# Kernel optimization log

Measured on AMD Instinct MI355X. Metric: run time of the kernel, lower is better.

The kernel has to match this reference:

```python
import jax, jax.numpy as jnp
import numpy as np

D_MODEL = 1024
H = 16
DK = D_MODEL // H
B, S = 2, 2048
NEG = -1e9


def setup_inputs() -> dict:
    key = jax.random.key(0)
    ks = jax.random.split(key, 7)
    scale = 1.0 / np.sqrt(D_MODEL)
    inp = {
        "q": jax.random.normal(ks[0], (B, S, D_MODEL), jnp.float32),
        "k": jax.random.normal(ks[1], (B, S, D_MODEL), jnp.float32),
        "v": jax.random.normal(ks[2], (B, S, D_MODEL), jnp.float32),
        # causal mask, broadcastable to (B, H, S, S); positions with 0 are masked
        "mask": jnp.tril(jnp.ones((S, S), dtype=bool))[None, None, :, :],
        "w_q": jax.random.normal(ks[3], (D_MODEL, D_MODEL), jnp.float32) * scale,
        "w_k": jax.random.normal(ks[4], (D_MODEL, D_MODEL), jnp.float32) * scale,
        "w_v": jax.random.normal(ks[5], (D_MODEL, D_MODEL), jnp.float32) * scale,
        "w_o": jax.random.normal(ks[6], (D_MODEL, D_MODEL), jnp.float32) * scale,
    }
    return inp


def reference(q, k, v, mask, w_q, w_k, w_v, w_o):
    # Linear projections (nn.Linear with bias=False: x @ W.T)
    query = q @ w_q.T  # (B, S, d_model)
    key_ = k @ w_k.T
    value = v @ w_v.T
    # split heads -> (B, h, S, dk)
    def split(x):
        return x.reshape(x.shape[0], x.shape[1], H, DK).transpose(0, 2, 1, 3)
    qh, kh, vh = split(query), split(key_), split(value)
    # scaled dot-product attention with full score materialization
    scores = jnp.einsum("bhqd,bhkd->bhqk", qh, kh) / jnp.sqrt(jnp.float32(DK))
    scores = jnp.where(mask, scores, NEG)
    attn = jax.nn.softmax(scores, axis=-1)  # (B, h, S, S); dropout p=0.0 -> identity
    out = jnp.einsum("bhqk,bhkd->bhqd", attn, vh)
    # merge heads -> (B, S, d_model)
    out = out.transpose(0, 2, 1, 3).reshape(out.shape[0], -1, H * DK)
    return out @ w_o.T
```

## Files before the change

### kernel.cpp

```cpp
#include <hip/hip_runtime.h>
#include <cstdint>
#include <cstddef>

typedef __bf16 bf16;
typedef __attribute__((ext_vector_type(4))) __bf16 bf16x4;
typedef __attribute__((ext_vector_type(8))) __bf16 bf16x8;
typedef __attribute__((ext_vector_type(4))) float floatx4;
typedef __attribute__((ext_vector_type(4))) short short4v;

#define MFMA16(a, b, c) __builtin_amdgcn_mfma_f32_16x16x32_bf16((a), (b), (c), 0, 0, 0)

__device__ __forceinline__ floatx4 MFMAK16(bf16x4 a, bf16x4 b, floatx4 c) {
#if __has_builtin(__builtin_amdgcn_mfma_f32_16x16x16bf16_1k)
  return __builtin_amdgcn_mfma_f32_16x16x16bf16_1k(
      __builtin_bit_cast(short4v, a), __builtin_bit_cast(short4v, b), c, 0, 0, 0);
#else
  floatx4 d;
  asm("v_mfma_f32_16x16x16_bf16 %0, %1, %2, %3"
      : "=v"(d)
      : "v"(a), "v"(b), "v"(c));
  return d;
#endif
}

constexpr int DMODEL = 1024;
constexpr int NH = 16;
constexpr int DKH = 64;
constexpr int B_ = 2;
constexpr int S_ = 2048;
constexpr int MTOT = B_ * S_;
constexpr float CEXP = 0.125f * 1.44269504f;

__device__ __forceinline__ void load_lds16(const void* g, void* l) {
  __builtin_amdgcn_global_load_lds(
      (const __attribute__((address_space(1))) uint32_t*)g,
      (__attribute__((address_space(3))) uint32_t*)l, 16, 0, 0);
}

__device__ __forceinline__ bf16x8 frag64(const bf16* lds, int row, int p) {
  int s = p ^ (row & 7);
  return *(const bf16x8*)&lds[row * 64 + s * 8];
}
__device__ __forceinline__ bf16x4 frag64h(const bf16* lds, int row, int p, int h) {
  int s = p ^ (row & 7);
  return *(const bf16x4*)&lds[row * 64 + s * 8 + h * 4];
}

__device__ __forceinline__ void stage32_bf16(const bf16* __restrict__ src,
                                             bf16* lds, int wave, int lane,
                                             int ldg) {
#pragma unroll
  for (int i = 0; i < 2; ++i) {
    int cb = (wave * 2 + i) * 64;
    int c = cb + lane;
    int r = c >> 2;
    int s = (c & 3) ^ ((r >> 1) & 3);
    load_lds16(&src[(size_t)r * ldg + s * 8], &lds[cb * 8]);
  }
}
__device__ __forceinline__ bf16x8 frag32_bf16(const bf16* lds, int row,
                                              int quad) {
  int s = quad ^ ((row >> 1) & 3);
  return *(const bf16x8*)&lds[row * 32 + s * 8];
}
__device__ __forceinline__ void stage32_f32(const float* __restrict__ src,
                                            float* lds, int wave, int lane,
                                            int ldg) {
#pragma unroll
  for (int i = 0; i < 4; ++i) {
    int cb = (wave * 4 + i) * 64;
    int c = cb + lane;
    int r = c >> 3;
    int s = (c & 7) ^ (r & 7);
    load_lds16(&src[(size_t)r * ldg + s * 4], &lds[cb * 4]);
  }
}
__device__ __forceinline__ bf16x8 frag32_f32(const float* lds, int row,
                                             int quad) {
  int s1 = (2 * quad) ^ (row & 7);
  int s2 = (2 * quad + 1) ^ (row & 7);
  float4 a = *(const float4*)&lds[row * 32 + s1 * 4];
  float4 b = *(const float4*)&lds[row * 32 + s2 * 4];
  bf16x8 h = {(bf16)a.x, (bf16)a.y, (bf16)a.z, (bf16)a.w,
              (bf16)b.x, (bf16)b.y, (bf16)b.z, (bf16)b.w};
  return h;
}

__global__ __launch_bounds__(256) void convert_kernel(
    const float* __restrict__ q, const float* __restrict__ k,
    const float* __restrict__ v, const float* __restrict__ wq,
    const float* __restrict__ wk, const float* __restrict__ wv,
    const float* __restrict__ wo, bf16* __restrict__ qb, bf16* __restrict__ kb,
    bf16* __restrict__ vb, bf16* __restrict__ wqb, bf16* __restrict__ wkb,
    bf16* __restrict__ wvb, bf16* __restrict__ wob) {
  const float* src;
  bf16* dst;
  size_t n;
  switch (blockIdx.y) {
    case 0: src = q;  dst = qb;  n = (size_t)MTOT * DMODEL; break;
    case 1: src = k;  dst = kb;  n = (size_t)MTOT * DMODEL; break;
    case 2: src = v;  dst = vb;  n = (size_t)MTOT * DMODEL; break;
    case 3: src = wq; dst = wqb; n = (size_t)DMODEL * DMODEL; break;
    case 4: src = wk; dst = wkb; n = (size_t)DMODEL * DMODEL; break;
    case 5: src = wv; dst = wvb; n = (size_t)DMODEL * DMODEL; break;
    default: src = wo; dst = wob; n = (size_t)DMODEL * DMODEL; break;
  }
  size_t idx = ((size_t)blockIdx.x * 256 + threadIdx.x) * 8;
  if (idx >= n) return;
  float4 f0 = *(const float4*)&src[idx];
  float4 f1 = *(const float4*)&src[idx + 4];
  bf16x8 h = {(bf16)f0.x, (bf16)f0.y, (bf16)f0.z, (bf16)f0.w,
              (bf16)f1.x, (bf16)f1.y, (bf16)f1.z, (bf16)f1.w};
  *(bf16x8*)&dst[idx] = h;
}

template <typename TC>
__device__ __forceinline__ void gemm64(const bf16* __restrict__ A,
                                       const bf16* __restrict__ W,
                                       TC* __restrict__ C,
                                       bf16* __restrict__ vt, int K,
                                       int m0, int n0, float ascale) {
  constexpr int N = DMODEL;
  __shared__ alignas(16) bf16 As[128 * 64];
  __shared__ alignas(16) bf16 Bs[128 * 64];

  const int tid = threadIdx.x;
  const int wave = tid >> 6;
  const int lane = tid & 63;
  const int quad = lane >> 4;
  const int l16 = lane & 15;
  const int wm = (wave >> 1) * 64;
  const int wn = (wave & 1) * 64;

  floatx4 acc[4][4] = {};

  for (int k0 = 0; k0 < K; k0 += 64) {
#pragma unroll
    for (int i = 0; i < 4; ++i) {
      int cb = (wave * 4 + i) * 64;
      int c = cb + lane;
      int r = c >> 3;
      int s = (c & 7) ^ (r & 7);
      load_lds16(&A[(size_t)(m0 + r) * K + k0 + s * 8], &As[cb * 8]);
      load_lds16(&W[(size_t)(n0 + r) * K + k0 + s * 8], &Bs[cb * 8]);
    }
    __syncthreads();

#pragma unroll
    for (int kk = 0; kk < 2; ++kk) {
      bf16x8 af[4], bfv[4];
#pragma unroll
      for (int mi = 0; mi < 4; ++mi)
        af[mi] = frag64(As, wm + mi * 16 + l16, kk * 4 + quad);
#pragma unroll
      for (int ni = 0; ni < 4; ++ni)
        bfv[ni] = frag64(Bs, wn + ni * 16 + l16, kk * 4 + quad);
#pragma unroll
      for (int mi = 0; mi < 4; ++mi)
#pragma unroll
        for (int ni = 0; ni < 4; ++ni)
          acc[mi][ni] = MFMA16(af[mi], bfv[ni], acc[mi][ni]);
    }
    __syncthreads();
  }

  if (vt) {
#pragma unroll
    for (int mi = 0; mi < 4; ++mi)
#pragma unroll
      for (int ni = 0; ni < 4; ++ni)
#pragma unroll
        for (int r = 0; r < 4; ++r) {
          int row = m0 + wm + mi * 16 + quad * 4 + r;
          int col = n0 + wn + ni * 16 + l16;
          int bb = row >> 11, s = row & 2047;
          int h = col >> 6, d = col & 63;
          vt[(size_t)((bb * NH + h) * DKH + d) * S_ + s] = (bf16)acc[mi][ni][r];
        }
  } else {
#pragma unroll
    for (int mi = 0; mi < 4; ++mi)
#pragma unroll
      for (int ni = 0; ni < 4; ++ni)
#pragma unroll
        for (int r = 0; r < 4; ++r) {
          int row = m0 + wm + mi * 16 + quad * 4 + r;
          int col = n0 + wn + ni * 16 + l16;
          C[(size_t)row * N + col] = (TC)(acc[mi][ni][r] * ascale);
        }
  }
}

__global__ __launch_bounds__(256, 3) void qkv64_kernel(
    const bf16* __restrict__ q, const bf16* __restrict__ k,
    const bf16* __restrict__ v, const bf16* __restrict__ wq,
    const bf16* __restrict__ wk, const bf16* __restrict__ wv,
    bf16* __restrict__ Q, bf16* __restrict__ K, bf16* __restrict__ Vt) {
  const int bid = blockIdx.x;
  const int xcd = bid & 7;
  const int j = bid >> 3;
  const int n = j & 7;
  const int rowslot = j >> 3;
  const int p = xcd * 12 + rowslot;
  const int z = p >> 5;
  const int y = p & 31;

  const bf16* A = (z == 0) ? q : (z == 1) ? k : v;
  const bf16* W = (z == 0) ? wq : (z == 1) ? wk : wv;
  bf16* C = (z == 0) ? Q : K;
  gemm64<bf16>(A, W, (z == 2) ? nullptr : C, (z == 2) ? Vt : nullptr,
               DMODEL, y * 128, n * 128, (z == 0) ? CEXP : 1.0f);
}

__global__ __launch_bounds__(256) void oproj64_kernel(
    const bf16* __restrict__ A, const bf16* __restrict__ W,
    float* __restrict__ C) {
  constexpr int K = DMODEL;
  constexpr int N = DMODEL;
  __shared__ alignas(16) bf16 As[64 * 64];
  __shared__ alignas(16) bf16 Bs[128 * 64];

  const int bid = blockIdx.x;
  const int xcd = bid & 7;
  const int j = bid >> 3;
  const int n = j & 7;
  const int slot = j >> 3;
  const int mt = xcd * 8 + slot;
  const int m0 = mt * 64;
  const int n0 = n * 128;

  const int tid = threadIdx.x;
  const int wave = tid >> 6;
  const int lane = tid & 63;
  const int quad = lane >> 4;
  const int l16 = lane & 15;
  const int wm = (wave >> 1) * 32;
  const int wn = (wave & 1) * 64;

  floatx4 acc[2][4] = {};

  for (int k0 = 0; k0 < K; k0 += 64) {
#pragma unroll
    for (int i = 0; i < 2; ++i) {
      int cb = (wave * 2 + i) * 64;
      int c = cb + lane;
      int r = c >> 3;
      int s = (c & 7) ^ (r & 7);
      load_lds16(&A[(size_t)(m0 + r) * K + k0 + s * 8], &As[cb * 8]);
    }
#pragma unroll
    for (int i = 0; i < 4; ++i) {
      int cb = (wave * 4 + i) * 64;
      int c = cb + lane;
      int r = c >> 3;
      int s = (c & 7) ^ (r & 7);
      load_lds16(&W[(size_t)(n0 + r) * K + k0 + s * 8], &Bs[cb * 8]);
    }
    __syncthreads();

#pragma unroll
    for (int kk = 0; kk < 2; ++kk) {
      bf16x8 af[2], bfv[4];
#pragma unroll
      for (int mi = 0; mi < 2; ++mi)
        af[mi] = frag64(As, wm + mi * 16 + l16, kk * 4 + quad);
#pragma unroll
      for (int ni = 0; ni < 4; ++ni)
        bfv[ni] = frag64(Bs, wn + ni * 16 + l16, kk * 4 + quad);
#pragma unroll
      for (int mi = 0; mi < 2; ++mi)
#pragma unroll
        for (int ni = 0; ni < 4; ++ni)
          acc[mi][ni] = MFMA16(af[mi], bfv[ni], acc[mi][ni]);
    }
    __syncthreads();
  }

#pragma unroll
  for (int mi = 0; mi < 2; ++mi)
#pragma unroll
    for (int ni = 0; ni < 4; ++ni)
#pragma unroll
      for (int r = 0; r < 4; ++r) {
        int row = m0 + wm + mi * 16 + quad * 4 + r;
        int col = n0 + wn + ni * 16 + l16;
        C[(size_t)row * N + col] = acc[mi][ni][r];
      }
}

template <typename TA, typename TW, typename TC>
__device__ __forceinline__ void gemm_core(const TA* __restrict__ A,
                                          const TW* __restrict__ W,
                                          TC* __restrict__ C,
                                          bf16* __restrict__ vt, int K,
                                          int m0, int n0, float ascale) {
  constexpr int N = DMODEL;
  __shared__ alignas(16) char smem[128 * 32 * (sizeof(TA) + sizeof(TW))];
  TA* As = (TA*)smem;
  TW* Bs = (TW*)(smem + 128 * 32 * sizeof(TA));

  const int tid = threadIdx.x;
  const int wave = tid >> 6;
  const int lane = tid & 63;
  const int quad = lane >> 4;
  const int l16 = lane & 15;
  const int wm = (wave >> 1) * 64;
  const int wn = (wave & 1) * 64;

  floatx4 acc[4][4] = {};

  for (int k0 = 0; k0 < K; k0 += 32) {
    if constexpr (sizeof(TA) == 2)
      stage32_bf16((const bf16*)A + (size_t)m0 * K + k0, (bf16*)As, wave, lane, K);
    else
      stage32_f32((const float*)A + (size_t)m0 * K + k0, (float*)As, wave, lane, K);
    if constexpr (sizeof(TW) == 2)
      stage32_bf16((const bf16*)W + (size_t)n0 * K + k0, (bf16*)Bs, wave, lane, K);
    else
      stage32_f32((const float*)W + (size_t)n0 * K + k0, (float*)Bs, wave, lane, K);
    __syncthreads();

    bf16x8 af[4], bfv[4];
#pragma unroll
    for (int mi = 0; mi < 4; ++mi) {
      if constexpr (sizeof(TA) == 2)
        af[mi] = frag32_bf16((const bf16*)As, wm + mi * 16 + l16, quad);
      else
        af[mi] = frag32_f32((const float*)As, wm + mi * 16 + l16, quad);
    }
#pragma unroll
    for (int ni = 0; ni < 4; ++ni) {
      if constexpr (sizeof(TW) == 2)
        bfv[ni] = frag32_bf16((const bf16*)Bs, wn + ni * 16 + l16, quad);
      else
        bfv[ni] = frag32_f32((const float*)Bs, wn + ni * 16 + l16, quad);
    }
#pragma unroll
    for (int mi = 0; mi < 4; ++mi)
#pragma unroll
      for (int ni = 0; ni < 4; ++ni)
        acc[mi][ni] = MFMA16(af[mi], bfv[ni], acc[mi][ni]);
    __syncthreads();
  }

  if (vt) {
#pragma unroll
    for (int mi = 0; mi < 4; ++mi)
#pragma unroll
      for (int ni = 0; ni < 4; ++ni)
#pragma unroll
        for (int r = 0; r < 4; ++r) {
          int row = m0 + wm + mi * 16 + quad * 4 + r;
          int col = n0 + wn + ni * 16 + l16;
          int bb = row >> 11, s = row & 2047;
          int h = col >> 6, d = col & 63;
          vt[(size_t)((bb * NH + h) * DKH + d) * S_ + s] = (bf16)acc[mi][ni][r];
        }
  } else {
#pragma unroll
    for (int mi = 0; mi < 4; ++mi)
#pragma unroll
      for (int ni = 0; ni < 4; ++ni)
#pragma unroll
        for (int r = 0; r < 4; ++r) {
          int row = m0 + wm + mi * 16 + quad * 4 + r;
          int col = n0 + wn + ni * 16 + l16;
          C[(size_t)row * N + col] = (TC)(acc[mi][ni][r] * ascale);
        }
  }
}

__global__ __launch_bounds__(256) void qkv_f32_kernel(
    const float* __restrict__ q, const float* __restrict__ k,
    const float* __restrict__ v, const float* __restrict__ wq,
    const float* __restrict__ wk, const float* __restrict__ wv,
    bf16* __restrict__ Q, bf16* __restrict__ K, bf16* __restrict__ Vt) {
  const int bid = blockIdx.x;
  const int xcd = bid & 7;
  const int j = bid >> 3;
  const int n = j & 7;
  const int rowslot = j >> 3;
  const int p = xcd * 12 + rowslot;
  const int z = p >> 5;
  const int y = p & 31;
  const float* A = (z == 0) ? q : (z == 1) ? k : v;
  const float* W = (z == 0) ? wq : (z == 1) ? wk : wv;
  bf16* C = (z == 0) ? Q : K;
  gemm_core<float, float, bf16>(A, W, (z == 2) ? nullptr : C,
                                (z == 2) ? Vt : nullptr, DMODEL, y * 128,
                                n * 128, (z == 0) ? CEXP : 1.0f);
}

__global__ __launch_bounds__(256) void oproj_f32_kernel(
    const bf16* __restrict__ A, const float* __restrict__ W,
    float* __restrict__ C) {
  const int bid = blockIdx.x;
  const int xcd = bid & 7;
  const int j = bid >> 3;
  const int n = j & 7;
  const int rowslot = j >> 3;
  const int y = xcd * 4 + rowslot;
  gemm_core<bf16, float, float>(A, W, C, nullptr, DMODEL, y * 128, n * 128,
                                1.0f);
}

__device__ __forceinline__ void stage_kv(const bf16* __restrict__ K,
                                         const bf16* __restrict__ Vt,
                                         bf16* Ks, bf16* Vts, size_t baseQ,
                                         size_t baseV, int kt, int wave,
                                         int lane) {
#pragma unroll
  for (int i = 0; i < 2; ++i) {
    int cb = (wave * 2 + i) * 64;
    int c = cb + lane;
    int r = c >> 3;
    int s = (c & 7) ^ (r & 7);
    load_lds16(&K[baseQ + (size_t)(kt * 64 + r) * DMODEL + s * 8], &Ks[cb * 8]);
    load_lds16(&Vt[baseV + (size_t)r * S_ + kt * 64 + s * 8], &Vts[cb * 8]);
  }
}

template <bool DIAG>
__device__ __forceinline__ void softmax4(const floatx4 sa[4], bf16x4 pb[4],
                                         float lp[4], int quad, int qb) {
#pragma unroll
  for (int kg = 0; kg < 4; ++kg) {
    float pv[4];
#pragma unroll
    for (int r = 0; r < 4; ++r) {
      float s = sa[kg][r];
      if (DIAG) {
        int key = kg * 16 + quad * 4 + r;
        s = (key > qb) ? -3.0e38f : s;
      }
      float p = __builtin_amdgcn_exp2f(s);
      lp[kg] += p;
      pv[r] = p;
    }
    pb[kg] = bf16x4{(bf16)pv[0], (bf16)pv[1], (bf16)pv[2], (bf16)pv[3]};
  }
}

template <bool DIAG>
__device__ __forceinline__ void attn_tile(const bf16* Ks, const bf16* Vts,
                                          const bf16x8 qf[2], floatx4 ot[4],
                                          float lp[4], int quad, int l16,
                                          int qb) {
  floatx4 sa[4] = {};
#pragma unroll
  for (int kk = 0; kk < 2; ++kk)
#pragma unroll
    for (int kg = 0; kg < 4; ++kg) {
      bf16x8 ka = frag64(Ks, kg * 16 + l16, kk * 4 + quad);
      sa[kg] = MFMA16(ka, qf[kk], sa[kg]);
    }
  bf16x4 pb[4];
  softmax4<DIAG>(sa, pb, lp, quad, qb);
#pragma unroll
  for (int kg = 0; kg < 4; ++kg)
#pragma unroll
    for (int di = 0; di < 4; ++di) {
      bf16x4 va = frag64h(Vts, di * 16 + l16, kg * 2 + (quad >> 1), quad & 1);
      ot[di] = MFMAK16(va, pb[kg], ot[di]);
    }
}

template <int LMODE>
__device__ __forceinline__ void pair_tile(const bf16* Ks, const bf16* Vts,
                                          const bf16x8 qfL[2],
                                          const bf16x8 qfH[2], floatx4 otL[4],
                                          floatx4 otH[4], float lpL[4],
                                          float lpH[4], int quad, int l16,
                                          int qb) {
  floatx4 saL[4] = {}, saH[4] = {};
#pragma unroll
  for (int kk = 0; kk < 2; ++kk)
#pragma unroll
    for (int kg = 0; kg < 4; ++kg) {
      bf16x8 ka = frag64(Ks, kg * 16 + l16, kk * 4 + quad);
      saL[kg] = MFMA16(ka, qfL[kk], saL[kg]);
      saH[kg] = MFMA16(ka, qfH[kk], saH[kg]);
    }
  bf16x4 pbL[4], pbH[4];
  if (LMODE == 1)
    softmax4<false>(saL, pbL, lpL, quad, qb);
  else
    softmax4<true>(saL, pbL, lpL, quad, qb);
  softmax4<false>(saH, pbH, lpH, quad, qb);
#pragma unroll
  for (int kg = 0; kg < 4; ++kg)
#pragma unroll
    for (int di = 0; di < 4; ++di) {
      bf16x4 va = frag64h(Vts, di * 16 + l16, kg * 2 + (quad >> 1), quad & 1);
      otL[di] = MFMAK16(va, pbL[kg], otL[di]);
      otH[di] = MFMAK16(va, pbH[kg], otH[di]);
    }
}

__global__ __launch_bounds__(256) void attn8_kernel(const bf16* __restrict__ Q,
                                                    const bf16* __restrict__ K,
                                                    const bf16* __restrict__ Vt,
                                                    bf16* __restrict__ O) {
  __shared__ alignas(16) bf16 Ks[2][64 * 64];
  __shared__ alignas(16) bf16 Vts[2][64 * 64];

  const int tid = threadIdx.x;
  const int wave = tid >> 6;
  const int lane = tid & 63;
  const int quad = lane >> 4;
  const int l16 = lane & 15;

  const int j = blockIdx.x;
  const int bh = j & 31;
  const int pr = j >> 5;
  const int qtL = pr;
  const int qtH = 31 - pr;
  const int h = bh & 15;
  const int b = bh >> 4;
  const size_t baseQ = (size_t)b * S_ * DMODEL + (size_t)h * DKH;
  const size_t baseV = (size_t)bh * DKH * S_;

  bf16x8 qfL[2], qfH[2];
#pragma unroll
  for (int kk = 0; kk < 2; ++kk) {
    qfL[kk] = *(const bf16x8*)&Q[baseQ +
        (size_t)(qtL * 64 + wave * 16 + l16) * DMODEL + kk * 32 + quad * 8];
    qfH[kk] = *(const bf16x8*)&Q[baseQ +
        (size_t)(qtH * 64 + wave * 16 + l16) * DMODEL + kk * 32 + quad * 8];
  }

  floatx4 otL[4] = {}, otH[4] = {};
  float lpL[4] = {}, lpH[4] = {};
  const int qb = wave * 16 + l16;

  stage_kv(K, Vt, Ks[0], Vts[0], baseQ, baseV, 0, wave, lane);
  __syncthreads();

  for (int kt = 0; kt < qtH; ++kt) {
    const int cur = kt & 1;
    stage_kv(K, Vt, Ks[cur ^ 1], Vts[cur ^ 1], baseQ, baseV, kt + 1, wave, lane);

    __builtin_amdgcn_s_setprio(1);
    if (kt < qtL)
      pair_tile<1>(Ks[cur], Vts[cur], qfL, qfH, otL, otH, lpL, lpH, quad, l16, qb);
    else if (kt == qtL)
      pair_tile<2>(Ks[cur], Vts[cur], qfL, qfH, otL, otH, lpL, lpH, quad, l16, qb);
    else
      attn_tile<false>(Ks[cur], Vts[cur], qfH, otH, lpH, quad, l16, qb);
    __builtin_amdgcn_s_setprio(0);

    __syncthreads();
  }
  {
    const int cur = qtH & 1;
    attn_tile<true>(Ks[cur], Vts[cur], qfH, otH, lpH, quad, l16, qb);
  }

  float lL = (lpL[0] + lpL[1]) + (lpL[2] + lpL[3]);
  lL += __shfl_xor(lL, 16, 64);
  lL += __shfl_xor(lL, 32, 64);
  float lH = (lpH[0] + lpH[1]) + (lpH[2] + lpH[3]);
  lH += __shfl_xor(lH, 16, 64);
  lH += __shfl_xor(lH, 32, 64);
  const float invL = 1.0f / lL;
  const float invH = 1.0f / lH;

  const size_t orowL = baseQ + (size_t)(qtL * 64 + wave * 16 + l16) * DMODEL;
  const size_t orowH = baseQ + (size_t)(qtH * 64 + wave * 16 + l16) * DMODEL;
#pragma unroll
  for (int di = 0; di < 4; ++di)
#pragma unroll
    for (int r = 0; r < 4; ++r) {
      O[orowL + di * 16 + quad * 4 + r] = (bf16)(otL[di][r] * invL);
      O[orowH + di * 16 + quad * 4 + r] = (bf16)(otH[di][r] * invH);
    }
}

extern "C" void kernel_launch(void* const* d_in, const int* in_sizes, int n_in,
                              void* d_out, int out_size, void* d_ws,
                              size_t ws_size, hipStream_t stream) {
  const float* q = (const float*)d_in[0];
  const float* k = (const float*)d_in[1];
  const float* v = (const float*)d_in[2];
  const float* wq = (const float*)d_in[4];
  const float* wk = (const float*)d_in[5];
  const float* wv = (const float*)d_in[6];
  const float* wo = (const float*)d_in[7];
  float* out = (float*)d_out;

  const size_t MB = 1024 * 1024;
  char* base = (char*)d_ws;
  bf16* Qp = (bf16*)(base);
  bf16* Kp = (bf16*)(base + 8 * MB);
  bf16* VtG = (bf16*)(base + 16 * MB);
  bf16* AO = (bf16*)(base + 24 * MB);

  if (ws_size >= 64 * MB) {
    bf16* qb = (bf16*)(base + 32 * MB);
    bf16* kb = (bf16*)(base + 40 * MB);
    bf16* vb = (bf16*)(base + 48 * MB);
    bf16* wqb = (bf16*)(base + 56 * MB);
    bf16* wkb = (bf16*)(base + 58 * MB);
    bf16* wvb = (bf16*)(base + 60 * MB);
    bf16* wob = (bf16*)(base + 62 * MB);
    convert_kernel<<<dim3(2048, 7), 256, 0, stream>>>(
        q, k, v, wq, wk, wv, wo, qb, kb, vb, wqb, wkb, wvb, wob);
    qkv64_kernel<<<dim3(768), 256, 0, stream>>>(
        qb, kb, vb, wqb, wkb, wvb, Qp, Kp, VtG);
    attn8_kernel<<<dim3(512), 256, 0, stream>>>(Qp, Kp, VtG, AO);
    oproj64_kernel<<<dim3(512), 256, 0, stream>>>(AO, wob, out);
  } else {
    qkv_f32_kernel<<<dim3(768), 256, 0, stream>>>(
        q, k, v, wq, wk, wv, Qp, Kp, VtG);
    attn8_kernel<<<dim3(512), 256, 0, stream>>>(Qp, Kp, VtG, AO);
    oproj_f32_kernel<<<dim3(256), 256, 0, stream>>>(AO, wo, out);
  }
}
```

Before: 209.5 us.

## Split attention KV loop across two wave groups with LDS reduction

The attention kernel now runs 8 waves per block instead of 4. Each pair of waves handles the same 16 query rows, and the two waves in a pair take alternating 64-key tiles, so two KV tiles are staged per iteration and the serial loop length is roughly halved. At the end, the partial output accumulators and row sums are combined through shared memory before normalization and the store. This doubles LDS use per block and adds a reduction step and an extra barrier, in exchange for more parallelism along the key dimension for the long causal rows.

```diff
diff --git a/kernel.cpp b/kernel.cpp
--- a/kernel.cpp
+++ b/kernel.cpp
@@ -404,19 +404,25 @@
                                 1.0f);
 }
 
-__device__ __forceinline__ void stage_kv(const bf16* __restrict__ K,
-                                         const bf16* __restrict__ Vt,
-                                         bf16* Ks, bf16* Vts, size_t baseQ,
-                                         size_t baseV, int kt, int wave,
-                                         int lane) {
-#pragma unroll
-  for (int i = 0; i < 2; ++i) {
-    int cb = (wave * 2 + i) * 64;
+__device__ __forceinline__ void stage_pair(const bf16* __restrict__ K,
+                                           const bf16* __restrict__ Vt,
+                                           bf16* Ksb, bf16* Vtsb, size_t baseQ,
+                                           size_t baseV, int kb, int wave,
+                                           int lane) {
+  const int p = wave & 1;
+  const int sub = wave >> 1;
+  const int kt = 2 * kb + p;
+  bf16* kd = Ksb + p * 4096;
+  bf16* vd = Vtsb + p * 4096;
+#pragma unroll
+  for (int ii = 0; ii < 2; ++ii) {
+    int i = sub * 2 + ii;
+    int cb = i * 64;
     int c = cb + lane;
     int r = c >> 3;
     int s = (c & 7) ^ (r & 7);
-    load_lds16(&K[baseQ + (size_t)(kt * 64 + r) * DMODEL + s * 8], &Ks[cb * 8]);
-    load_lds16(&Vt[baseV + (size_t)r * S_ + kt * 64 + s * 8], &Vts[cb * 8]);
+    load_lds16(&K[baseQ + (size_t)(kt * 64 + r) * DMODEL + s * 8], &kd[cb * 8]);
+    load_lds16(&Vt[baseV + (size_t)r * S_ + kt * 64 + s * 8], &vd[cb * 8]);
   }
 }
 
@@ -497,18 +503,19 @@
     }
 }
 
-__global__ __launch_bounds__(256) void attn8_kernel(const bf16* __restrict__ Q,
-                                                    const bf16* __restrict__ K,
-                                                    const bf16* __restrict__ Vt,
-                                                    bf16* __restrict__ O) {
-  __shared__ alignas(16) bf16 Ks[2][64 * 64];
-  __shared__ alignas(16) bf16 Vts[2][64 * 64];
+__global__ __launch_bounds__(512, 4) void attn10_kernel(
+    const bf16* __restrict__ Q, const bf16* __restrict__ K,
+    const bf16* __restrict__ Vt, bf16* __restrict__ O) {
+  __shared__ alignas(16) bf16 Ks[2][2 * 64 * 64];
+  __shared__ alignas(16) bf16 Vts[2][2 * 64 * 64];
 
   const int tid = threadIdx.x;
   const int wave = tid >> 6;
   const int lane = tid & 63;
   const int quad = lane >> 4;
   const int l16 = lane & 15;
+  const int ws = wave >> 1;
+  const int kh = wave & 1;
 
   const int j = blockIdx.x;
   const int bh = j & 31;
@@ -524,56 +531,90 @@
 #pragma unroll
   for (int kk = 0; kk < 2; ++kk) {
     qfL[kk] = *(const bf16x8*)&Q[baseQ +
-        (size_t)(qtL * 64 + wave * 16 + l16) * DMODEL + kk * 32 + quad * 8];
+        (size_t)(qtL * 64 + ws * 16 + l16) * DMODEL + kk * 32 + quad * 8];
     qfH[kk] = *(const bf16x8*)&Q[baseQ +
-        (size_t)(qtH * 64 + wave * 16 + l16) * DMODEL + kk * 32 + quad * 8];
+        (size_t)(qtH * 64 + ws * 16 + l16) * DMODEL + kk * 32 + quad * 8];
   }
 
   floatx4 otL[4] = {}, otH[4] = {};
   float lpL[4] = {}, lpH[4] = {};
-  const int qb = wave * 16 + l16;
-
-  stage_kv(K, Vt, Ks[0], Vts[0], baseQ, baseV, 0, wave, lane);
+  const int qb = ws * 16 + l16;
+
+  const int NSI = (33 - pr) >> 1;
+
+  stage_pair(K, Vt, Ks[0], Vts[0], baseQ, baseV, 0, wave, lane);
   __syncthreads();
 
-  for (int kt = 0; kt < qtH; ++kt) {
-    const int cur = kt & 1;
-    stage_kv(K, Vt, Ks[cur ^ 1], Vts[cur ^ 1], baseQ, baseV, kt + 1, wave, lane);
-
+  for (int kb = 0; kb < NSI; ++kb) {
+    const int cur = kb & 1;
+    if (kb + 1 < NSI)
+      stage_pair(K, Vt, Ks[cur ^ 1], Vts[cur ^ 1], baseQ, baseV, kb + 1, wave, lane);
+
+    const int kt = 2 * kb + kh;
     __builtin_amdgcn_s_setprio(1);
-    if (kt < qtL)
-      pair_tile<1>(Ks[cur], Vts[cur], qfL, qfH, otL, otH, lpL, lpH, quad, l16, qb);
-    else if (kt == qtL)
-      pair_tile<2>(Ks[cur], Vts[cur], qfL, qfH, otL, otH, lpL, lpH, quad, l16, qb);
-    else
-      attn_tile<false>(Ks[cur], Vts[cur], qfH, otH, lpH, quad, l16, qb);
+    if (kt <= qtH) {
+      const bf16* ks = Ks[cur] + kh * 4096;
+      const bf16* vs = Vts[cur] + kh * 4096;
+      if (kt < qtL)
+        pair_tile<1>(ks, vs, qfL, qfH, otL, otH, lpL, lpH, quad, l16, qb);
+      else if (kt == qtL)
+        pair_tile<2>(ks, vs, qfL, qfH, otL, otH, lpL, lpH, quad, l16, qb);
+      else if (kt == qtH)
+        attn_tile<true>(ks, vs, qfH, otH, lpH, quad, l16, qb);
+      else
+        attn_tile<false>(ks, vs, qfH, otH, lpH, quad, l16, qb);
+    }
     __builtin_amdgcn_s_setprio(0);
 
     __syncthreads();
   }
-  {
-    const int cur = qtH & 1;
-    attn_tile<true>(Ks[cur], Vts[cur], qfH, otH, lpH, quad, l16, qb);
-  }
-
-  float lL = (lpL[0] + lpL[1]) + (lpL[2] + lpL[3]);
-  lL += __shfl_xor(lL, 16, 64);
-  lL += __shfl_xor(lL, 32, 64);
-  float lH = (lpH[0] + lpH[1]) + (lpH[2] + lpH[3]);
-  lH += __shfl_xor(lH, 16, 64);
-  lH += __shfl_xor(lH, 32, 64);
-  const float invL = 1.0f / lL;
-  const float invH = 1.0f / lH;
-
-  const size_t orowL = baseQ + (size_t)(qtL * 64 + wave * 16 + l16) * DMODEL;
-  const size_t orowH = baseQ + (size_t)(qtH * 64 + wave * 16 + l16) * DMODEL;
-#pragma unroll
-  for (int di = 0; di < 4; ++di)
-#pragma unroll
-    for (int r = 0; r < 4; ++r) {
-      O[orowL + di * 16 + quad * 4 + r] = (bf16)(otL[di][r] * invL);
-      O[orowH + di * 16 + quad * 4 + r] = (bf16)(otH[di][r] * invH);
-    }
+
+  floatx4* ox = (floatx4*)&Ks[0][0];
+  float* lx = (float*)&Vts[0][0];
+  if (kh == 1) {
+#pragma unroll
+    for (int di = 0; di < 4; ++di) {
+      ox[((ws * 2 + 0) * 4 + di) * 64 + lane] = otL[di];
+      ox[((ws * 2 + 1) * 4 + di) * 64 + lane] = otH[di];
+    }
+#pragma unroll
+    for (int kg = 0; kg < 4; ++kg) {
+      lx[((ws * 2 + 0) * 4 + kg) * 64 + lane] = lpL[kg];
+      lx[((ws * 2 + 1) * 4 + kg) * 64 + lane] = lpH[kg];
+    }
+  }
+  __syncthreads();
+  if (kh == 0) {
+#pragma unroll
+    for (int di = 0; di < 4; ++di) {
+      otL[di] += ox[((ws * 2 + 0) * 4 + di) * 64 + lane];
+      otH[di] += ox[((ws * 2 + 1) * 4 + di) * 64 + lane];
+    }
+#pragma unroll
+    for (int kg = 0; kg < 4; ++kg) {
+      lpL[kg] += lx[((ws * 2 + 0) * 4 + kg) * 64 + lane];
+      lpH[kg] += lx[((ws * 2 + 1) * 4 + kg) * 64 + lane];
+    }
+
+    float lL = (lpL[0] + lpL[1]) + (lpL[2] + lpL[3]);
+    lL += __shfl_xor(lL, 16, 64);
+    lL += __shfl_xor(lL, 32, 64);
+    float lH = (lpH[0] + lpH[1]) + (lpH[2] + lpH[3]);
+    lH += __shfl_xor(lH, 16, 64);
+    lH += __shfl_xor(lH, 32, 64);
+    const float invL = 1.0f / lL;
+    const float invH = 1.0f / lH;
+
+    const size_t orowL = baseQ + (size_t)(qtL * 64 + ws * 16 + l16) * DMODEL;
+    const size_t orowH = baseQ + (size_t)(qtH * 64 + ws * 16 + l16) * DMODEL;
+#pragma unroll
+    for (int di = 0; di < 4; ++di)
+#pragma unroll
+      for (int r = 0; r < 4; ++r) {
+        O[orowL + di * 16 + quad * 4 + r] = (bf16)(otL[di][r] * invL);
+        O[orowH + di * 16 + quad * 4 + r] = (bf16)(otH[di][r] * invH);
+      }
+  }
 }
 
 extern "C" void kernel_launch(void* const* d_in, const int* in_sizes, int n_in,
@@ -607,12 +648,12 @@
         q, k, v, wq, wk, wv, wo, qb, kb, vb, wqb, wkb, wvb, wob);
     qkv64_kernel<<<dim3(768), 256, 0, stream>>>(
         qb, kb, vb, wqb, wkb, wvb, Qp, Kp, VtG);
-    attn8_kernel<<<dim3(512), 256, 0, stream>>>(Qp, Kp, VtG, AO);
+    attn10_kernel<<<dim3(512), 512, 0, stream>>>(Qp, Kp, VtG, AO);
     oproj64_kernel<<<dim3(512), 256, 0, stream>>>(AO, wob, out);
   } else {
     qkv_f32_kernel<<<dim3(768), 256, 0, stream>>>(
         q, k, v, wq, wk, wv, Qp, Kp, VtG);
-    attn8_kernel<<<dim3(512), 256, 0, stream>>>(Qp, Kp, VtG, AO);
+    attn10_kernel<<<dim3(512), 512, 0, stream>>>(Qp, Kp, VtG, AO);
     oproj_f32_kernel<<<dim3(256), 256, 0, stream>>>(AO, wo, out);
   }
 }
```

Result: faster. 203.4 us (-2.9%).

## Stage V-transpose epilogue through LDS and switch output projection to 128x128 tiles

Applied to the files above, without the earlier changes.

The V projection epilogue previously wrote each bf16 element of the transposed V scattered across strided rows of global memory. It now writes the tile transposed into padded shared memory and then emits contiguous 16-byte row segments to global memory. The output projection drops its custom 64x128 kernel and reuses the 128x128 gemm64 tile with 256 blocks, which gives more reuse per block but fewer blocks to fill the GPU. The shared buffer grows slightly to hold the padded transpose.

```diff
diff --git a/kernel.cpp b/kernel.cpp
--- a/kernel.cpp
+++ b/kernel.cpp
@@ -121,8 +121,9 @@
                                        bf16* __restrict__ vt, int K,
                                        int m0, int n0, float ascale) {
   constexpr int N = DMODEL;
-  __shared__ alignas(16) bf16 As[128 * 64];
-  __shared__ alignas(16) bf16 Bs[128 * 64];
+  __shared__ alignas(16) bf16 smem[128 * 136];
+  bf16* As = smem;
+  bf16* Bs = smem + 128 * 64;
 
   const int tid = threadIdx.x;
   const int wave = tid >> 6;
@@ -165,18 +166,28 @@
   }
 
   if (vt) {
+    bf16* T = smem;
 #pragma unroll
     for (int mi = 0; mi < 4; ++mi)
 #pragma unroll
-      for (int ni = 0; ni < 4; ++ni)
-#pragma unroll
-        for (int r = 0; r < 4; ++r) {
-          int row = m0 + wm + mi * 16 + quad * 4 + r;
-          int col = n0 + wn + ni * 16 + l16;
-          int bb = row >> 11, s = row & 2047;
-          int h = col >> 6, d = col & 63;
-          vt[(size_t)((bb * NH + h) * DKH + d) * S_ + s] = (bf16)acc[mi][ni][r];
-        }
+      for (int ni = 0; ni < 4; ++ni) {
+        int row = wm + mi * 16 + quad * 4;
+        int col = wn + ni * 16 + l16;
+        bf16x4 vvv = {(bf16)acc[mi][ni][0], (bf16)acc[mi][ni][1],
+                      (bf16)acc[mi][ni][2], (bf16)acc[mi][ni][3]};
+        *(bf16x4*)&T[col * 136 + row] = vvv;
+      }
+    __syncthreads();
+    const int bb = m0 >> 11;
+    const int sbase = (m0 & 2047) + l16 * 8;
+#pragma unroll
+    for (int jj = 0; jj < 8; ++jj) {
+      int colv = wave * 32 + jj * 4 + quad;
+      int gcol = n0 + colv;
+      int h = gcol >> 6, d = gcol & 63;
+      bf16x8 rowv = *(const bf16x8*)&T[colv * 136 + l16 * 8];
+      *(bf16x8*)&vt[(size_t)((bb * NH + h) * DKH + d) * S_ + sbase] = rowv;
+    }
   } else {
 #pragma unroll
     for (int mi = 0; mi < 4; ++mi)
@@ -212,80 +223,16 @@
                DMODEL, y * 128, n * 128, (z == 0) ? CEXP : 1.0f);
 }
 
-__global__ __launch_bounds__(256) void oproj64_kernel(
+__global__ __launch_bounds__(256) void oproj128_kernel(
     const bf16* __restrict__ A, const bf16* __restrict__ W,
     float* __restrict__ C) {
-  constexpr int K = DMODEL;
-  constexpr int N = DMODEL;
-  __shared__ alignas(16) bf16 As[64 * 64];
-  __shared__ alignas(16) bf16 Bs[128 * 64];
-
   const int bid = blockIdx.x;
   const int xcd = bid & 7;
   const int j = bid >> 3;
   const int n = j & 7;
   const int slot = j >> 3;
-  const int mt = xcd * 8 + slot;
-  const int m0 = mt * 64;
-  const int n0 = n * 128;
-
-  const int tid = threadIdx.x;
-  const int wave = tid >> 6;
-  const int lane = tid & 63;
-  const int quad = lane >> 4;
-  const int l16 = lane & 15;
-  const int wm = (wave >> 1) * 32;
-  const int wn = (wave & 1) * 64;
-
-  floatx4 acc[2][4] = {};
-
-  for (int k0 = 0; k0 < K; k0 += 64) {
-#pragma unroll
-    for (int i = 0; i < 2; ++i) {
-      int cb = (wave * 2 + i) * 64;
-      int c = cb + lane;
-      int r = c >> 3;
-      int s = (c & 7) ^ (r & 7);
-      load_lds16(&A[(size_t)(m0 + r) * K + k0 + s * 8], &As[cb * 8]);
-    }
-#pragma unroll
-    for (int i = 0; i < 4; ++i) {
-      int cb = (wave * 4 + i) * 64;
-      int c = cb + lane;
-      int r = c >> 3;
-      int s = (c & 7) ^ (r & 7);
-      load_lds16(&W[(size_t)(n0 + r) * K + k0 + s * 8], &Bs[cb * 8]);
-    }
-    __syncthreads();
-
-#pragma unroll
-    for (int kk = 0; kk < 2; ++kk) {
-      bf16x8 af[2], bfv[4];
-#pragma unroll
-      for (int mi = 0; mi < 2; ++mi)
-        af[mi] = frag64(As, wm + mi * 16 + l16, kk * 4 + quad);
-#pragma unroll
-      for (int ni = 0; ni < 4; ++ni)
-        bfv[ni] = frag64(Bs, wn + ni * 16 + l16, kk * 4 + quad);
-#pragma unroll
-      for (int mi = 0; mi < 2; ++mi)
-#pragma unroll
-        for (int ni = 0; ni < 4; ++ni)
-          acc[mi][ni] = MFMA16(af[mi], bfv[ni], acc[mi][ni]);
-    }
-    __syncthreads();
-  }
-
-#pragma unroll
-  for (int mi = 0; mi < 2; ++mi)
-#pragma unroll
-    for (int ni = 0; ni < 4; ++ni)
-#pragma unroll
-      for (int r = 0; r < 4; ++r) {
-        int row = m0 + wm + mi * 16 + quad * 4 + r;
-        int col = n0 + wn + ni * 16 + l16;
-        C[(size_t)row * N + col] = acc[mi][ni][r];
-      }
+  gemm64<float>(A, W, C, nullptr, DMODEL, (xcd * 4 + slot) * 128, n * 128,
+                1.0f);
 }
 
 template <typename TA, typename TW, typename TC>
@@ -608,7 +555,7 @@
     qkv64_kernel<<<dim3(768), 256, 0, stream>>>(
         qb, kb, vb, wqb, wkb, wvb, Qp, Kp, VtG);
     attn8_kernel<<<dim3(512), 256, 0, stream>>>(Qp, Kp, VtG, AO);
-    oproj64_kernel<<<dim3(512), 256, 0, stream>>>(AO, wob, out);
+    oproj128_kernel<<<dim3(256), 256, 0, stream>>>(AO, wob, out);
   } else {
     qkv_f32_kernel<<<dim3(768), 256, 0, stream>>>(
         q, k, v, wq, wk, wv, Qp, Kp, VtG);
```

After: 206.9 us. About the same (-1.2%).

## Narrow QKV GEMM tiles to 128x64, stage V-transpose through LDS, compact convert grid

Applied to the files above, without the earlier changes.

The QKV projection GEMM switches from 128x128 to 128x64 output tiles, doubling the block count to 1536 and raising the occupancy hint to 4 blocks per CU, with a new XCD-aware block mapping. The transposed V write now goes through a padded LDS tile so each lane stores 16-byte contiguous runs instead of scattered 2-byte stores. The convert kernel drops its 2D grid, which had many idle blocks for the small weight segments, in favour of a compact 1D grid with no out-of-range early exits. Narrower tiles reduce reuse of the A operand per block, which raises L2/global traffic.

```diff
diff --git a/kernel.cpp b/kernel.cpp
--- a/kernel.cpp
+++ b/kernel.cpp
@@ -93,20 +93,28 @@
     const float* __restrict__ wo, bf16* __restrict__ qb, bf16* __restrict__ kb,
     bf16* __restrict__ vb, bf16* __restrict__ wqb, bf16* __restrict__ wkb,
     bf16* __restrict__ wvb, bf16* __restrict__ wob) {
+  const int bid = blockIdx.x;
+  int seg, rel;
+  if (bid < 6144) {
+    seg = bid >> 11;
+    rel = bid & 2047;
+  } else {
+    int t = bid - 6144;
+    seg = 3 + (t >> 9);
+    rel = t & 511;
+  }
   const float* src;
   bf16* dst;
-  size_t n;
-  switch (blockIdx.y) {
-    case 0: src = q;  dst = qb;  n = (size_t)MTOT * DMODEL; break;
-    case 1: src = k;  dst = kb;  n = (size_t)MTOT * DMODEL; break;
-    case 2: src = v;  dst = vb;  n = (size_t)MTOT * DMODEL; break;
-    case 3: src = wq; dst = wqb; n = (size_t)DMODEL * DMODEL; break;
-    case 4: src = wk; dst = wkb; n = (size_t)DMODEL * DMODEL; break;
-    case 5: src = wv; dst = wvb; n = (size_t)DMODEL * DMODEL; break;
-    default: src = wo; dst = wob; n = (size_t)DMODEL * DMODEL; break;
-  }
-  size_t idx = ((size_t)blockIdx.x * 256 + threadIdx.x) * 8;
-  if (idx >= n) return;
+  switch (seg) {
+    case 0: src = q;  dst = qb;  break;
+    case 1: src = k;  dst = kb;  break;
+    case 2: src = v;  dst = vb;  break;
+    case 3: src = wq; dst = wqb; break;
+    case 4: src = wk; dst = wkb; break;
+    case 5: src = wv; dst = wvb; break;
+    default: src = wo; dst = wob; break;
+  }
+  size_t idx = ((size_t)rel * 256 + threadIdx.x) * 8;
   float4 f0 = *(const float4*)&src[idx];
   float4 f1 = *(const float4*)&src[idx + 4];
   bf16x8 h = {(bf16)f0.x, (bf16)f0.y, (bf16)f0.z, (bf16)f0.w,
@@ -115,14 +123,15 @@
 }
 
 template <typename TC>
-__device__ __forceinline__ void gemm64(const bf16* __restrict__ A,
-                                       const bf16* __restrict__ W,
-                                       TC* __restrict__ C,
-                                       bf16* __restrict__ vt, int K,
-                                       int m0, int n0, float ascale) {
+__device__ __forceinline__ void gemm_bn64(const bf16* __restrict__ A,
+                                          const bf16* __restrict__ W,
+                                          TC* __restrict__ C,
+                                          bf16* __restrict__ vt, int K,
+                                          int m0, int n0, float ascale) {
   constexpr int N = DMODEL;
-  __shared__ alignas(16) bf16 As[128 * 64];
-  __shared__ alignas(16) bf16 Bs[128 * 64];
+  __shared__ alignas(16) bf16 smem[128 * 64 + 64 * 64];
+  bf16* As = smem;
+  bf16* Bs = smem + 128 * 64;
 
   const int tid = threadIdx.x;
   const int wave = tid >> 6;
@@ -130,9 +139,9 @@
   const int quad = lane >> 4;
   const int l16 = lane & 15;
   const int wm = (wave >> 1) * 64;
-  const int wn = (wave & 1) * 64;
-
-  floatx4 acc[4][4] = {};
+  const int wn = (wave & 1) * 32;
+
+  floatx4 acc[4][2] = {};
 
   for (int k0 = 0; k0 < K; k0 += 64) {
 #pragma unroll
@@ -142,46 +151,63 @@
       int r = c >> 3;
       int s = (c & 7) ^ (r & 7);
       load_lds16(&A[(size_t)(m0 + r) * K + k0 + s * 8], &As[cb * 8]);
+    }
+#pragma unroll
+    for (int i = 0; i < 2; ++i) {
+      int cb = (wave * 2 + i) * 64;
+      int c = cb + lane;
+      int r = c >> 3;
+      int s = (c & 7) ^ (r & 7);
       load_lds16(&W[(size_t)(n0 + r) * K + k0 + s * 8], &Bs[cb * 8]);
     }
     __syncthreads();
 
 #pragma unroll
     for (int kk = 0; kk < 2; ++kk) {
-      bf16x8 af[4], bfv[4];
+      bf16x8 af[4], bfv[2];
 #pragma unroll
       for (int mi = 0; mi < 4; ++mi)
         af[mi] = frag64(As, wm + mi * 16 + l16, kk * 4 + quad);
 #pragma unroll
-      for (int ni = 0; ni < 4; ++ni)
+      for (int ni = 0; ni < 2; ++ni)
         bfv[ni] = frag64(Bs, wn + ni * 16 + l16, kk * 4 + quad);
 #pragma unroll
       for (int mi = 0; mi < 4; ++mi)
 #pragma unroll
-        for (int ni = 0; ni < 4; ++ni)
+        for (int ni = 0; ni < 2; ++ni)
           acc[mi][ni] = MFMA16(af[mi], bfv[ni], acc[mi][ni]);
     }
     __syncthreads();
   }
 
   if (vt) {
+    bf16* T = smem;
 #pragma unroll
     for (int mi = 0; mi < 4; ++mi)
 #pragma unroll
-      for (int ni = 0; ni < 4; ++ni)
-#pragma unroll
-        for (int r = 0; r < 4; ++r) {
-          int row = m0 + wm + mi * 16 + quad * 4 + r;
-          int col = n0 + wn + ni * 16 + l16;
-          int bb = row >> 11, s = row & 2047;
-          int h = col >> 6, d = col & 63;
-          vt[(size_t)((bb * NH + h) * DKH + d) * S_ + s] = (bf16)acc[mi][ni][r];
-        }
+      for (int ni = 0; ni < 2; ++ni) {
+        int row = wm + mi * 16 + quad * 4;
+        int col = wn + ni * 16 + l16;
+        bf16x4 vvv = {(bf16)acc[mi][ni][0], (bf16)acc[mi][ni][1],
+                      (bf16)acc[mi][ni][2], (bf16)acc[mi][ni][3]};
+        *(bf16x4*)&T[col * 136 + row] = vvv;
+      }
+    __syncthreads();
+    const int bb = m0 >> 11;
+    const int sbase = (m0 & 2047) + l16 * 8;
+#pragma unroll
+    for (int jj = 0; jj < 4; ++jj) {
+      int colv = wave * 16 + jj * 4 + quad;
+      int gcol = n0 + colv;
+      int h = gcol >> 6, d = gcol & 63;
+      bf16x8 rowv = *(const bf16x8*)&T[colv * 136 + l16 * 8];
+      *(bf16x8*)&vt[(size_t)((bb * NH + h) * DKH + d) * S_ + sbase] = rowv;
+    }
   } else {
 #pragma unroll
     for (int mi = 0; mi < 4; ++mi)
 #pragma unroll
-      for (int ni = 0; ni < 4; ++ni)
+      for (int ni = 0; ni < 2; ++ni)
 #pragma unroll
         for (int r = 0; r < 4; ++r) {
           int row = m0 + wm + mi * 16 + quad * 4 + r;
@@ -191,25 +217,25 @@
   }
 }
 
-__global__ __launch_bounds__(256, 3) void qkv64_kernel(
+__global__ __launch_bounds__(256, 4) void qkv64_kernel(
     const bf16* __restrict__ q, const bf16* __restrict__ k,
     const bf16* __restrict__ v, const bf16* __restrict__ wq,
     const bf16* __restrict__ wk, const bf16* __restrict__ wv,
     bf16* __restrict__ Q, bf16* __restrict__ K, bf16* __restrict__ Vt) {
   const int bid = blockIdx.x;
   const int xcd = bid & 7;
-  const int j = bid >> 3;
-  const int n = j & 7;
-  const int rowslot = j >> 3;
-  const int p = xcd * 12 + rowslot;
-  const int z = p >> 5;
-  const int y = p & 31;
+  const int idx = bid >> 3;
+  const int z = idx >> 6;
+  const int rem = idx & 63;
+  const int n = rem & 15;
+  const int yslot = rem >> 4;
+  const int y = xcd * 4 + yslot;
 
   const bf16* A = (z == 0) ? q : (z == 1) ? k : v;
   const bf16* W = (z == 0) ? wq : (z == 1) ? wk : wv;
   bf16* C = (z == 0) ? Q : K;
-  gemm64<bf16>(A, W, (z == 2) ? nullptr : C, (z == 2) ? Vt : nullptr,
-               DMODEL, y * 128, n * 128, (z == 0) ? CEXP : 1.0f);
+  gemm_bn64<bf16>(A, W, (z == 2) ? nullptr : C, (z == 2) ? Vt : nullptr,
+                  DMODEL, y * 128, n * 64, (z == 0) ? CEXP : 1.0f);
 }
 
 __global__ __launch_bounds__(256) void oproj64_kernel(
@@ -603,9 +629,9 @@
     bf16* wkb = (bf16*)(base + 58 * MB);
     bf16* wvb = (bf16*)(base + 60 * MB);
     bf16* wob = (bf16*)(base + 62 * MB);
-    convert_kernel<<<dim3(2048, 7), 256, 0, stream>>>(
+    convert_kernel<<<dim3(8192), 256, 0, stream>>>(
         q, k, v, wq, wk, wv, wo, qb, kb, vb, wqb, wkb, wvb, wob);
-    qkv64_kernel<<<dim3(768), 256, 0, stream>>>(
+    qkv64_kernel<<<dim3(1536), 256, 0, stream>>>(
         qb, kb, vb, wqb, wkb, wvb, Qp, Kp, VtG);
     attn8_kernel<<<dim3(512), 256, 0, stream>>>(Qp, Kp, VtG, AO);
     oproj64_kernel<<<dim3(512), 256, 0, stream>>>(AO, wob, out);
```

After: 205.5 us. Within noise of the previous version (-1.9%).
